# Kernel optimization log

Hardware: AMD Instinct MI355X
Metric: run time of the kernel (lower is better)

The kernel has to match this reference:

```python
import jax, jax.numpy as jnp
import numpy as np

HEADS = 4
DIM_HEAD = 32
SCALE = 16.0
EPS = 1e-5  # jax.nn.standardize default


def _standardize(t):
    # standardize over last axis (the flattened x*y*z sequence), per (b, h, d)
    mu = jnp.mean(t, axis=-1, keepdims=True)
    var = jnp.var(t, axis=-1, keepdims=True)
    return (t - mu) * jax.lax.rsqrt(var + EPS)


def setup_inputs() -> dict:
    key = jax.random.key(0)
    k1, k2, k3 = jax.random.split(key, 3)
    dim = 64
    hidden = HEADS * DIM_HEAD  # 128
    b, x, y, z = 2, 16, 16, 16
    inp = jax.random.normal(k1, (b, x, y, z, dim), dtype=jnp.float32)
    # 1x1x1 convs == pointwise channel matmuls; init like flax lecun_normal-ish scale
    w_qkv = jax.random.normal(k2, (dim, 3 * hidden), dtype=jnp.float32) / np.sqrt(dim)
    w_out = jax.random.normal(k3, (hidden, dim), dtype=jnp.float32) / np.sqrt(hidden)
    b_out = jnp.zeros((dim,), dtype=jnp.float32)
    return {"input": inp, "w_qkv": w_qkv, "w_out": w_out, "b_out": b_out}


def reference(input, w_qkv, w_out, b_out):
    b, x, y, z, c = input.shape
    s = x * y * z
    # pointwise conv -> qkv
    qkv = jnp.einsum('bxyzc,cd->bxyzd', input, w_qkv)  # [b,x,y,z,3*hidden]
    q, k, v = jnp.split(qkv, 3, axis=-1)
    # rearrange 'b x y z (h c) -> b h c (x y z)'
    def to_bhds(t):
        return t.reshape(b, s, HEADS, DIM_HEAD).transpose(0, 2, 3, 1)  # [b,h,d,s]
    q, k, v = map(to_bhds, (q, k, v))
    q = _standardize(q)
    k = _standardize(k)
    sim = jnp.einsum('bhdi,bhdj->bhij', q, k) * SCALE  # [b,h,s,s]
    attn = jax.nn.softmax(sim, axis=-1)
    out = jnp.einsum('bhij,bhdj->bhid', attn, v)  # [b,h,s,d]
    # rearrange 'b h (x y z) d -> b x y z (h d)'
    out = out.transpose(0, 2, 1, 3).reshape(b, x, y, z, HEADS * DIM_HEAD)
    return jnp.einsum('bxyzc,co->bxyzo', out, w_out) + b_out
```

## Files before the change

kernel.cpp:

```cpp
#include <hip/hip_runtime.h>
#include <math.h>
#include <stdint.h>


typedef __attribute__((ext_vector_type(8))) short short8;
typedef __attribute__((ext_vector_type(4))) float f32x4;
typedef __attribute__((ext_vector_type(16))) float f32x16;

#define QSCALE 23.083120654223414f

#if __has_builtin(__builtin_amdgcn_exp2f)
#define EXP2F(x) __builtin_amdgcn_exp2f(x)
#else
#define EXP2F(x) exp2f(x)
#endif

__device__ inline uint32_t pack_hilo(float y) {
  uint32_t uy = __float_as_uint(y);
  uint32_t hb = (uy + 0x7fffu + ((uy >> 16) & 1u)) >> 16;
  float hf = __uint_as_float(hb << 16);
  float r = y - hf;
  uint32_t ur = __float_as_uint(r);
  uint32_t lb = (ur + 0x7fffu + ((ur >> 16) & 1u)) >> 16;
  return (hb << 16) | (lb & 0xffffu);
}

__device__ inline ushort f32_to_bf16(float y) {
  uint32_t uy = __float_as_uint(y);
  return (ushort)((uy + 0x7fffu + ((uy >> 16) & 1u)) >> 16);
}

__device__ inline float bpermf(int addr, float v) {
  return __int_as_float(__builtin_amdgcn_ds_bpermute(addr, __float_as_int(v)));
}

__device__ inline short8 as_s8(uint4 v) {
  union { uint4 u; short8 s; } t;
  t.u = v;
  return t.s;
}

__global__ __launch_bounds__(256) void qkv_kernel(const float* __restrict__ in,
                                                  const float* __restrict__ w,
                                                  float* __restrict__ qf,
                                                  float* __restrict__ kf,
                                                  ushort* __restrict__ vfr,
                                                  float* __restrict__ psum,
                                                  float* __restrict__ psq) {
  __shared__ char smem[18432];
  __shared__ float ssum[64], ssq[64];
  ushort* Bh = (ushort*)smem;
  ushort* Bl = (ushort*)(smem + 9216);
  float* VT = (float*)smem;

  const int ctile = blockIdx.x % 6;
  const int stile = blockIdx.x / 6;
  const int tid = threadIdx.x;
  const int row0 = stile * 64;
  const int sel = ctile >> 1;

  if (tid < 64) { ssum[tid] = 0.f; ssq[tid] = 0.f; }

  {
    const int col = tid & 63;
    const int k0 = (tid >> 6) * 16;
    const float* wp = w + (size_t)k0 * 384 + ctile * 64 + col;
    float xv[16];
#pragma unroll
    for (int j = 0; j < 16; ++j) xv[j] = wp[(size_t)j * 384];
    uint32_t hi[8], lo[8];
#pragma unroll
    for (int p = 0; p < 8; ++p) {
      const uint32_t u0 = __float_as_uint(xv[2 * p]);
      const uint32_t u1 = __float_as_uint(xv[2 * p + 1]);
      hi[p] = __builtin_amdgcn_perm(u1, u0, 0x07060302u);
      const float d0 = xv[2 * p] - __uint_as_float(u0 & 0xffff0000u);
      const float d1 = xv[2 * p + 1] - __uint_as_float(u1 & 0xffff0000u);
      lo[p] = __builtin_amdgcn_perm(__float_as_uint(d1), __float_as_uint(d0), 0x07060302u);
    }
    uint4* bh = (uint4*)&Bh[col * 72 + k0];
    bh[0] = make_uint4(hi[0], hi[1], hi[2], hi[3]);
    bh[1] = make_uint4(hi[4], hi[5], hi[6], hi[7]);
    uint4* bl = (uint4*)&Bl[col * 72 + k0];
    bl[0] = make_uint4(lo[0], lo[1], lo[2], lo[3]);
    bl[1] = make_uint4(lo[4], lo[5], lo[6], lo[7]);
  }
  __syncthreads();

  const int wv = tid >> 6, lane = tid & 63;
  const int wr = wv >> 1, wc = wv & 1;
  const int h2 = lane >> 5, pl = lane & 31;

  short8 ah[4], al[4];
  {
    const float* ap = in + (size_t)(row0 + wr * 32 + pl) * 64 + h2 * 8;
#pragma unroll
    for (int kb = 0; kb < 4; ++kb) {
      const float4 xa = *(const float4*)(ap + kb * 16);
      const float4 xb = *(const float4*)(ap + kb * 16 + 4);
      const float xs[8] = {xa.x, xa.y, xa.z, xa.w, xb.x, xb.y, xb.z, xb.w};
      uint32_t hp[4], lp[4];
#pragma unroll
      for (int p = 0; p < 4; ++p) {
        const uint32_t u0 = __float_as_uint(xs[2 * p]);
        const uint32_t u1 = __float_as_uint(xs[2 * p + 1]);
        hp[p] = __builtin_amdgcn_perm(u1, u0, 0x07060302u);
        const float d0 = xs[2 * p] - __uint_as_float(u0 & 0xffff0000u);
        const float d1 = xs[2 * p + 1] - __uint_as_float(u1 & 0xffff0000u);
        lp[p] = __builtin_amdgcn_perm(__float_as_uint(d1), __float_as_uint(d0), 0x07060302u);
      }
      union { uint32_t u[4]; short8 s; } th, tl;
      th.u[0] = hp[0]; th.u[1] = hp[1]; th.u[2] = hp[2]; th.u[3] = hp[3];
      tl.u[0] = lp[0]; tl.u[1] = lp[1]; tl.u[2] = lp[2]; tl.u[3] = lp[3];
      ah[kb] = th.s;
      al[kb] = tl.s;
    }
  }

  const ushort* bhp = &Bh[(wc * 32 + pl) * 72 + h2 * 8];
  const ushort* blp = &Bl[(wc * 32 + pl) * 72 + h2 * 8];
  f32x16 acc = {};
#pragma unroll
  for (int kb = 0; kb < 4; ++kb) {
    const short8 bh = *(const short8*)(bhp + kb * 16);
    const short8 bl = *(const short8*)(blp + kb * 16);
    acc = __builtin_amdgcn_mfma_f32_32x32x16_bf16(ah[kb], bh, acc, 0, 0, 0);
    acc = __builtin_amdgcn_mfma_f32_32x32x16_bf16(ah[kb], bl, acc, 0, 0, 0);
    acc = __builtin_amdgcn_mfma_f32_32x32x16_bf16(al[kb], bh, acc, 0, 0, 0);
  }

  const int b = row0 >> 12;
  const int sl0 = (row0 & 4095) + wr * 32;
  const int chg = ctile * 64 + wc * 32 + pl;

  if (sel < 2) {
    const int hd0 = chg & 127;
    const int h = hd0 >> 5, d0 = hd0 & 31;
    float* dst = (sel == 0 ? qf : kf) + ((size_t)(b * 4 + h) * 4096 + sl0) * 32 + d0;
    float s1 = 0.f, s2 = 0.f;
#pragma unroll
    for (int reg = 0; reg < 16; ++reg) {
      const int r = (reg & 3) + 8 * (reg >> 2) + 4 * h2;
      dst[(size_t)r * 32] = acc[reg];
      s1 += acc[reg];
      s2 += acc[reg] * acc[reg];
    }
    atomicAdd(&ssum[wc * 32 + pl], s1);
    atomicAdd(&ssq[wc * 32 + pl], s2);
    __syncthreads();
    if (tid < 64) {
      const int ch = (ctile & 1) * 64 + tid;
      const int idx = (((sel * 2 + b) * 128) + ch) * 64 + (stile & 63);
      psum[idx] = ssum[tid];
      psq[idx] = ssq[tid];
    }
  } else {
    __syncthreads();
    const int chv = wc * 32 + pl;
#pragma unroll
    for (int reg = 0; reg < 16; ++reg) {
      const int r = wr * 32 + (reg & 3) + 8 * (reg >> 2) + 4 * h2;
      VT[chv * 68 + r] = acc[reg];
    }
    __syncthreads();
    const int jt0 = (row0 & 4095) >> 5;
#pragma unroll
    for (int hl = 0; hl < 2; ++hl) {
      const int jtl = tid >> 7, c = (tid >> 6) & 1, ln = tid & 63;
      const int d = ln & 31, hh = ln >> 5;
      const int jloc = 32 * jtl + 16 * c + 8 * hh;
      const int ch = hl * 32 + d;
      const float4 f0 = *(const float4*)&VT[ch * 68 + jloc];
      const float4 f1 = *(const float4*)&VT[ch * 68 + jloc + 4];
      uint4 pk;
      pk.x = (uint32_t)f32_to_bf16(f0.x) | ((uint32_t)f32_to_bf16(f0.y) << 16);
      pk.y = (uint32_t)f32_to_bf16(f0.z) | ((uint32_t)f32_to_bf16(f0.w) << 16);
      pk.z = (uint32_t)f32_to_bf16(f1.x) | ((uint32_t)f32_to_bf16(f1.y) << 16);
      pk.w = (uint32_t)f32_to_bf16(f1.z) | ((uint32_t)f32_to_bf16(f1.w) << 16);
      const int h = (ctile - 4) * 2 + hl;
      ushort* dst =
          vfr + (((size_t)((b * 4 + h) * 128 + jt0 + jtl) * 2 + c) * 64 + ln) * 8;
      *(uint4*)dst = pk;
    }
  }
}

__global__ __launch_bounds__(256) void norm_kernel(const float* __restrict__ qf,
                                                   const float* __restrict__ kf,
                                                   ushort* __restrict__ qfr_hi,
                                                   ushort* __restrict__ qfr_lo,
                                                   ushort* __restrict__ kfr_hi,
                                                   ushort* __restrict__ kfr_lo,
                                                   const float* __restrict__ psum,
                                                   const float* __restrict__ psq) {
  const int bx = blockIdx.x;
  const int tensor = bx >> 7;
  const int bh = (bx >> 4) & 7;
  const int s0 = (bx & 15) * 256;
  const int tid = threadIdx.x;
  __shared__ float red[2][32][8];
  __shared__ float tA[32], tB[32];
  {
    const int d = tid >> 3, p = tid & 7;
    const int base = ((tensor * 2 + (bh >> 2)) * 128 + (bh & 3) * 32 + d) * 64 + p * 8;
    float sm = 0.f, sq = 0.f;
#pragma unroll
    for (int e = 0; e < 8; ++e) {
      sm += psum[base + e];
      sq += psq[base + e];
    }
    red[0][d][p] = sm;
    red[1][d][p] = sq;
  }
  __syncthreads();
  if (tid < 32) {
    float sm = 0.f, sq = 0.f;
#pragma unroll
    for (int e = 0; e < 8; ++e) {
      sm += red[0][tid][e];
      sq += red[1][tid][e];
    }
    const float mu = sm * (1.f / 4096.f);
    const float scale = tensor == 0 ? QSCALE : 1.0f;
    const float inv = rsqrtf(sq * (1.f / 4096.f) - mu * mu + 1e-5f) * scale;
    tA[tid] = inv;
    tB[tid] = -mu * inv;
  }
  __syncthreads();

  const float* src = (tensor == 0 ? qf : kf) + (size_t)bh * 4096 * 32;
  ushort* dhi = (tensor == 0 ? qfr_hi : kfr_hi) + (size_t)(bh * 128 + (s0 >> 5)) * 1024;
  ushort* dlo = (tensor == 0 ? qfr_lo : kfr_lo) + (size_t)(bh * 128 + (s0 >> 5)) * 1024;
#pragma unroll
  for (int pass = 0; pass < 4; ++pass) {
    const int idx = tid + pass * 256;
    const int jtl = idx >> 7;
    const int c = (idx >> 6) & 1;
    const int ln = idx & 63;
    const int p = ln & 31, hh = ln >> 5;
    const int row = tensor == 0 ? p : ((p & 0x13) | ((p & 4) << 1) | ((p & 8) >> 1));
    const int s = s0 + 32 * jtl + row;
    const int d0 = 16 * c + 8 * hh;
    const float4 x0 = *(const float4*)&src[(size_t)s * 32 + d0];
    const float4 x1 = *(const float4*)&src[(size_t)s * 32 + d0 + 4];
    const float4 A0 = *(const float4*)&tA[d0];
    const float4 A1 = *(const float4*)&tA[d0 + 4];
    const float4 B0 = *(const float4*)&tB[d0];
    const float4 B1 = *(const float4*)&tB[d0 + 4];
    uint32_t pk[8];
    pk[0] = pack_hilo(fmaf(x0.x, A0.x, B0.x));
    pk[1] = pack_hilo(fmaf(x0.y, A0.y, B0.y));
    pk[2] = pack_hilo(fmaf(x0.z, A0.z, B0.z));
    pk[3] = pack_hilo(fmaf(x0.w, A0.w, B0.w));
    pk[4] = pack_hilo(fmaf(x1.x, A1.x, B1.x));
    pk[5] = pack_hilo(fmaf(x1.y, A1.y, B1.y));
    pk[6] = pack_hilo(fmaf(x1.z, A1.z, B1.z));
    pk[7] = pack_hilo(fmaf(x1.w, A1.w, B1.w));
    uint4 HV, LV;
    HV.x = __builtin_amdgcn_perm(pk[1], pk[0], 0x07060302u);
    HV.y = __builtin_amdgcn_perm(pk[3], pk[2], 0x07060302u);
    HV.z = __builtin_amdgcn_perm(pk[5], pk[4], 0x07060302u);
    HV.w = __builtin_amdgcn_perm(pk[7], pk[6], 0x07060302u);
    LV.x = __builtin_amdgcn_perm(pk[1], pk[0], 0x05040100u);
    LV.y = __builtin_amdgcn_perm(pk[3], pk[2], 0x05040100u);
    LV.z = __builtin_amdgcn_perm(pk[5], pk[4], 0x05040100u);
    LV.w = __builtin_amdgcn_perm(pk[7], pk[6], 0x05040100u);
    const size_t doff = ((size_t)(jtl * 2 + c) * 64 + ln) * 8;
    *(uint4*)(dhi + doff) = HV;
    *(uint4*)(dlo + doff) = LV;
  }
}

__global__ __launch_bounds__(512, 4) void attn_kernel(const ushort* __restrict__ qfr_hi,
                                                      const ushort* __restrict__ qfr_lo,
                                                      const ushort* __restrict__ kfr_hi,
                                                      const ushort* __restrict__ kfr_lo,
                                                      const ushort* __restrict__ vfr,
                                                      float* __restrict__ o) {
  __shared__ float OM[8 * 32 * 36];
  __shared__ float ML[8 * 64];

  const int tid = threadIdx.x;
  const int w = tid >> 6;
  const int js = w & 3;
  const int itl = w >> 2;
  const int lane = tid & 63;
  const int pl = lane & 31, h2 = lane >> 5;
  const int bh = blockIdx.x & 7;
  const int itp = blockIdx.x >> 3;
  const int it = itp * 2 + itl;

  const size_t qbase = (size_t)(bh * 128 + it) * 1024 + lane * 8;
  const short8 qh0 = *(const short8*)(qfr_hi + qbase);
  const short8 qh1 = *(const short8*)(qfr_hi + qbase + 512);
  const short8 ql0 = *(const short8*)(qfr_lo + qbase);
  const short8 ql1 = *(const short8*)(qfr_lo + qbase + 512);

  const int bp32 = (lane ^ 32) << 2;

  const size_t kbase = (size_t)(bh * 128 + js * 32) * 1024 + lane * 8;
  const ushort* kh = kfr_hi + kbase;
  const ushort* kl = kfr_lo + kbase;
  const ushort* vp = vfr + kbase;

  f32x16 oacc;
#pragma unroll
  for (int r = 0; r < 16; ++r) oacc[r] = 0.f;
  const f32x16 zf = {};
  float m = -INFINITY, l = 0.f;

  uint4 rk0 = *(const uint4*)(kh);
  uint4 rk1 = *(const uint4*)(kh + 512);
  uint4 rl0 = *(const uint4*)(kl);
  uint4 rl1 = *(const uint4*)(kl + 512);
  uint4 rv0 = *(const uint4*)(vp);
  uint4 rv1 = *(const uint4*)(vp + 512);

  for (int t = 0; t < 32; ++t) {
    const short8 ck0 = as_s8(rk0), ck1 = as_s8(rk1);
    const short8 cl0 = as_s8(rl0), cl1 = as_s8(rl1);
    const short8 cv0 = as_s8(rv0), cv1 = as_s8(rv1);
    {
      const int off = (t + 1) * 1024;
      rk0 = *(const uint4*)(kh + off);
      rk1 = *(const uint4*)(kh + off + 512);
      rl0 = *(const uint4*)(kl + off);
      rl1 = *(const uint4*)(kl + off + 512);
      rv0 = *(const uint4*)(vp + off);
      rv1 = *(const uint4*)(vp + off + 512);
    }

    __builtin_amdgcn_s_setprio(1);
    f32x16 sc = __builtin_amdgcn_mfma_f32_32x32x16_bf16(ck0, qh0, zf, 0, 0, 0);
    sc = __builtin_amdgcn_mfma_f32_32x32x16_bf16(ck1, qh1, sc, 0, 0, 0);
    sc = __builtin_amdgcn_mfma_f32_32x32x16_bf16(ck0, ql0, sc, 0, 0, 0);
    sc = __builtin_amdgcn_mfma_f32_32x32x16_bf16(ck1, ql1, sc, 0, 0, 0);
    sc = __builtin_amdgcn_mfma_f32_32x32x16_bf16(cl0, qh0, sc, 0, 0, 0);
    sc = __builtin_amdgcn_mfma_f32_32x32x16_bf16(cl1, qh1, sc, 0, 0, 0);
    __builtin_amdgcn_s_setprio(0);

    const float x0 = fmaxf(fmaxf(sc[0], sc[1]), sc[2]);
    const float x1 = fmaxf(fmaxf(sc[3], sc[4]), sc[5]);
    const float x2 = fmaxf(fmaxf(sc[6], sc[7]), sc[8]);
    const float x3 = fmaxf(fmaxf(sc[9], sc[10]), sc[11]);
    const float x4 = fmaxf(fmaxf(sc[12], sc[13]), sc[14]);
    float mx = fmaxf(fmaxf(fmaxf(x0, x1), x2), fmaxf(fmaxf(x3, x4), sc[15]));
    mx = fmaxf(mx, bpermf(bp32, mx));
    const float mn = fmaxf(m, mx);
    const float al = EXP2F(m - mn);
    m = mn;
#pragma unroll
    for (int r = 0; r < 16; ++r) sc[r] = EXP2F(sc[r] - mn);
    float rs = 0.f;
#pragma unroll
    for (int r = 0; r < 16; ++r) rs += sc[r];
    rs += bpermf(bp32, rs);
    l = l * al + rs;
#pragma unroll
    for (int r = 0; r < 16; ++r) oacc[r] *= al;

    uint32_t pk[8];
#pragma unroll
    for (int i = 0; i < 8; ++i)
      pk[i] = __builtin_amdgcn_perm(__float_as_uint(sc[2 * i + 1]),
                                    __float_as_uint(sc[2 * i]), 0x07060302u);
    union { uint32_t u4[4]; short8 s8; } p0, p1;
    p0.u4[0] = pk[0]; p0.u4[1] = pk[1]; p0.u4[2] = pk[2]; p0.u4[3] = pk[3];
    p1.u4[0] = pk[4]; p1.u4[1] = pk[5]; p1.u4[2] = pk[6]; p1.u4[3] = pk[7];

    __builtin_amdgcn_s_setprio(1);
    oacc = __builtin_amdgcn_mfma_f32_32x32x16_bf16(cv0, p0.s8, oacc, 0, 0, 0);
    oacc = __builtin_amdgcn_mfma_f32_32x32x16_bf16(cv1, p1.s8, oacc, 0, 0, 0);
    __builtin_amdgcn_s_setprio(0);
  }

  {
    float* om = OM + (size_t)(w * 32 + pl) * 36;
#pragma unroll
    for (int g = 0; g < 4; ++g)
      *(float4*)&om[4 * h2 + 8 * g] =
          make_float4(oacc[4 * g], oacc[4 * g + 1], oacc[4 * g + 2], oacc[4 * g + 3]);
    if (h2 == 0) {
      ML[w * 64 + pl] = m;
      ML[w * 64 + 32 + pl] = l;
    }
  }
  __syncthreads();
  const int b = bh >> 2, h = bh & 3;
#pragma unroll
  for (int pass = 0; pass < 4; ++pass) {
    const int idx = tid + pass * 512;
    const int itl2 = idx >> 10;
    const int i = (idx >> 5) & 31;
    const int d = idx & 31;
    const int wb = itl2 * 4;
    const float m0 = ML[(wb + 0) * 64 + i], m1 = ML[(wb + 1) * 64 + i];
    const float m2 = ML[(wb + 2) * 64 + i], m3 = ML[(wb + 3) * 64 + i];
    const float l0 = ML[(wb + 0) * 64 + 32 + i], l1 = ML[(wb + 1) * 64 + 32 + i];
    const float l2 = ML[(wb + 2) * 64 + 32 + i], l3 = ML[(wb + 3) * 64 + 32 + i];
    const float M = fmaxf(fmaxf(m0, m1), fmaxf(m2, m3));
    const float w0 = EXP2F(m0 - M), w1 = EXP2F(m1 - M);
    const float w2 = EXP2F(m2 - M), w3 = EXP2F(m3 - M);
    const float L = l0 * w0 + l1 * w1 + l2 * w2 + l3 * w3;
    const float val = (OM[((wb + 0) * 32 + i) * 36 + d] * w0 +
                       OM[((wb + 1) * 32 + i) * 36 + d] * w1 +
                       OM[((wb + 2) * 32 + i) * 36 + d] * w2 +
                       OM[((wb + 3) * 32 + i) * 36 + d] * w3) *
                      (1.001953125f / L);
    const int ig = (itp * 2 + itl2) * 32 + i;
    o[((size_t)(b * 4096) + ig) * 128 + h * 32 + d] = val;
  }
}

__global__ __launch_bounds__(256) void proj_kernel(const float* __restrict__ o,
                                                   const float* __restrict__ w,
                                                   const float* __restrict__ bias,
                                                   float* __restrict__ out) {
  __shared__ float wT[64 * 132];
  const int tid = threadIdx.x;
  for (int idx = tid; idx < 8192; idx += 256) {
    const int c = idx >> 6, col = idx & 63;
    const int g = (c >> 2) ^ ((col >> 3) & 7);
    wT[col * 132 + (g << 2) + (c & 3)] = w[idx];
  }
  __syncthreads();
  const int col = tid & 63;
  const int r = blockIdx.x * 8 + ((tid >> 6) << 1);
  const float* r0 = o + (size_t)r * 128;
  const float* r1 = r0 + 128;
  const int wbase = col * 132;
  const int gx = (col >> 3) & 7;
  float a0 = bias[col], a1 = a0;
  for (int c = 0; c < 128; c += 4) {
    const float4 x0 = *(const float4*)&r0[c];
    const float4 x1 = *(const float4*)&r1[c];
    const float4 wv = *(const float4*)&wT[wbase + ((((c >> 2) ^ gx)) << 2)];
    a0 = fmaf(x0.x, wv.x, a0); a0 = fmaf(x0.y, wv.y, a0);
    a0 = fmaf(x0.z, wv.z, a0); a0 = fmaf(x0.w, wv.w, a0);
    a1 = fmaf(x1.x, wv.x, a1); a1 = fmaf(x1.y, wv.y, a1);
    a1 = fmaf(x1.z, wv.z, a1); a1 = fmaf(x1.w, wv.w, a1);
  }
  out[(size_t)r * 64 + col] = a0;
  out[(size_t)(r + 1) * 64 + col] = a1;
}

extern "C" void kernel_launch(void* const* d_in, const int* in_sizes, int n_in,
                              void* d_out, int out_size, void* d_ws, size_t ws_size,
                              hipStream_t stream) {
  const float* input = (const float*)d_in[0];
  const float* w_qkv = (const float*)d_in[1];
  const float* w_out = (const float*)d_in[2];
  const float* b_out = (const float*)d_in[3];

  char* W = (char*)d_ws;
  float* qf = (float*)(W + 0);
  float* kf = (float*)(W + (4u << 20));
  ushort* kfr_hi = (ushort*)(W + (8u << 20));
  ushort* kfr_lo = (ushort*)(W + (10u << 20));
  ushort* vfr = (ushort*)(W + (12u << 20));
  ushort* qfr_hi = (ushort*)(W + (14u << 20));
  ushort* qfr_lo = (ushort*)(W + (16u << 20));
  float* psum = (float*)(W + (18u << 20));
  float* psq = (float*)(W + (18u << 20) + (128u << 10));
  float* ob = qf;
  float* out = (float*)d_out;

  hipLaunchKernelGGL(qkv_kernel, dim3(768), dim3(256), 0, stream, input, w_qkv, qf, kf,
                     vfr, psum, psq);
  hipLaunchKernelGGL(norm_kernel, dim3(256), dim3(256), 0, stream, qf, kf, qfr_hi,
                     qfr_lo, kfr_hi, kfr_lo, psum, psq);
  hipLaunchKernelGGL(attn_kernel, dim3(512), dim3(512), 0, stream, qfr_hi, qfr_lo,
                     kfr_hi, kfr_lo, vfr, ob);
  hipLaunchKernelGGL(proj_kernel, dim3(1024), dim3(256), 0, stream, ob, w_out, b_out, out);
}
```

Before: 131.7 us.

## Split attention KV range across 8 waves per query tile and double grid

Each block now handles one 32-row query tile with all 8 waves splitting the key sequence into 16-tile chunks. Previously each block handled two query tiles with 4 waves each over 32 key tiles. The grid doubles to 1024 blocks and the final merge combines 8 partial softmax states instead of 4. Launch bounds raise the occupancy hint to 8, and the row-sum is rewritten as a tree reduction. The aim is more parallelism and shorter serial loops per wave, at the cost of more merge work and more redundant Q loads.

```diff
diff --git a/kernel.cpp b/kernel.cpp
--- a/kernel.cpp
+++ b/kernel.cpp
@@ -271,7 +271,7 @@
   }
 }
 
-__global__ __launch_bounds__(512, 4) void attn_kernel(const ushort* __restrict__ qfr_hi,
+__global__ __launch_bounds__(512, 8) void attn_kernel(const ushort* __restrict__ qfr_hi,
                                                       const ushort* __restrict__ qfr_lo,
                                                       const ushort* __restrict__ kfr_hi,
                                                       const ushort* __restrict__ kfr_lo,
@@ -282,13 +282,11 @@
 
   const int tid = threadIdx.x;
   const int w = tid >> 6;
-  const int js = w & 3;
-  const int itl = w >> 2;
+  const int js = w;
   const int lane = tid & 63;
   const int pl = lane & 31, h2 = lane >> 5;
   const int bh = blockIdx.x & 7;
-  const int itp = blockIdx.x >> 3;
-  const int it = itp * 2 + itl;
+  const int it = blockIdx.x >> 3;
 
   const size_t qbase = (size_t)(bh * 128 + it) * 1024 + lane * 8;
   const short8 qh0 = *(const short8*)(qfr_hi + qbase);
@@ -298,7 +296,7 @@
 
   const int bp32 = (lane ^ 32) << 2;
 
-  const size_t kbase = (size_t)(bh * 128 + js * 32) * 1024 + lane * 8;
+  const size_t kbase = (size_t)(bh * 128 + js * 16) * 1024 + lane * 8;
   const ushort* kh = kfr_hi + kbase;
   const ushort* kl = kfr_lo + kbase;
   const ushort* vp = vfr + kbase;
@@ -316,7 +314,7 @@
   uint4 rv0 = *(const uint4*)(vp);
   uint4 rv1 = *(const uint4*)(vp + 512);
 
-  for (int t = 0; t < 32; ++t) {
+  for (int t = 0; t < 16; ++t) {
     const short8 ck0 = as_s8(rk0), ck1 = as_s8(rk1);
     const short8 cl0 = as_s8(rl0), cl1 = as_s8(rl1);
     const short8 cv0 = as_s8(rv0), cv1 = as_s8(rv1);
@@ -351,9 +349,11 @@
     m = mn;
 #pragma unroll
     for (int r = 0; r < 16; ++r) sc[r] = EXP2F(sc[r] - mn);
-    float rs = 0.f;
-#pragma unroll
-    for (int r = 0; r < 16; ++r) rs += sc[r];
+    const float s0 = sc[0] + sc[1], s1 = sc[2] + sc[3];
+    const float s2 = sc[4] + sc[5], s3 = sc[6] + sc[7];
+    const float s4 = sc[8] + sc[9], s5 = sc[10] + sc[11];
+    const float s6 = sc[12] + sc[13], s7 = sc[14] + sc[15];
+    float rs = ((s0 + s1) + (s2 + s3)) + ((s4 + s5) + (s6 + s7));
     rs += bpermf(bp32, rs);
     l = l * al + rs;
 #pragma unroll
@@ -388,26 +388,28 @@
   __syncthreads();
   const int b = bh >> 2, h = bh & 3;
 #pragma unroll
-  for (int pass = 0; pass < 4; ++pass) {
+  for (int pass = 0; pass < 2; ++pass) {
     const int idx = tid + pass * 512;
-    const int itl2 = idx >> 10;
-    const int i = (idx >> 5) & 31;
+    const int i = idx >> 5;
     const int d = idx & 31;
-    const int wb = itl2 * 4;
-    const float m0 = ML[(wb + 0) * 64 + i], m1 = ML[(wb + 1) * 64 + i];
-    const float m2 = ML[(wb + 2) * 64 + i], m3 = ML[(wb + 3) * 64 + i];
-    const float l0 = ML[(wb + 0) * 64 + 32 + i], l1 = ML[(wb + 1) * 64 + 32 + i];
-    const float l2 = ML[(wb + 2) * 64 + 32 + i], l3 = ML[(wb + 3) * 64 + 32 + i];
-    const float M = fmaxf(fmaxf(m0, m1), fmaxf(m2, m3));
-    const float w0 = EXP2F(m0 - M), w1 = EXP2F(m1 - M);
-    const float w2 = EXP2F(m2 - M), w3 = EXP2F(m3 - M);
-    const float L = l0 * w0 + l1 * w1 + l2 * w2 + l3 * w3;
-    const float val = (OM[((wb + 0) * 32 + i) * 36 + d] * w0 +
-                       OM[((wb + 1) * 32 + i) * 36 + d] * w1 +
-                       OM[((wb + 2) * 32 + i) * 36 + d] * w2 +
-                       OM[((wb + 3) * 32 + i) * 36 + d] * w3) *
-                      (1.001953125f / L);
-    const int ig = (itp * 2 + itl2) * 32 + i;
+    float mk[8], lk[8];
+#pragma unroll
+    for (int k = 0; k < 8; ++k) {
+      mk[k] = ML[k * 64 + i];
+      lk[k] = ML[k * 64 + 32 + i];
+    }
+    const float M01 = fmaxf(mk[0], mk[1]), M23 = fmaxf(mk[2], mk[3]);
+    const float M45 = fmaxf(mk[4], mk[5]), M67 = fmaxf(mk[6], mk[7]);
+    const float M = fmaxf(fmaxf(M01, M23), fmaxf(M45, M67));
+    float L = 0.f, V = 0.f;
+#pragma unroll
+    for (int k = 0; k < 8; ++k) {
+      const float wk = EXP2F(mk[k] - M);
+      L += lk[k] * wk;
+      V += OM[(k * 32 + i) * 36 + d] * wk;
+    }
+    const float val = V * (1.001953125f / L);
+    const int ig = it * 32 + i;
     o[((size_t)(b * 4096) + ig) * 128 + h * 32 + d] = val;
   }
 }
@@ -469,7 +471,7 @@
                      vfr, psum, psq);
   hipLaunchKernelGGL(norm_kernel, dim3(256), dim3(256), 0, stream, qf, kf, qfr_hi,
                      qfr_lo, kfr_hi, kfr_lo, psum, psq);
-  hipLaunchKernelGGL(attn_kernel, dim3(512), dim3(512), 0, stream, qfr_hi, qfr_lo,
+  hipLaunchKernelGGL(attn_kernel, dim3(1024), dim3(512), 0, stream, qfr_hi, qfr_lo,
                      kfr_hi, kfr_lo, vfr, ob);
   hipLaunchKernelGGL(proj_kernel, dim3(1024), dim3(256), 0, stream, ob, w_out, b_out, out);
 }
```

After: 464.8 us. 253% more time.
